# Optimization experiments

Hardware: AMD Instinct MI355X
Metric: run time of the kernel (lower is better)

The kernel has to match this reference:

```python
import jax, jax.numpy as jnp
import numpy as np

BS, SEQ, DK = 4, 4096, 128

def setup_inputs() -> dict:
    key = jax.random.key(0)
    kq, kk, kv = jax.random.split(key, 3)
    q = jax.random.normal(kq, (BS, SEQ, DK), dtype=jnp.float32)
    k = jax.random.normal(kk, (BS, SEQ, DK), dtype=jnp.float32)
    v = jax.random.normal(kv, (BS, SEQ, DK), dtype=jnp.float32)
    return {"q": q, "k": k, "v": v}

def reference(q, k, v):
    d_k = q.shape[-1]
    # scores: [bs, s_q, s_k]
    scaled = jnp.einsum('bqd,bkd->bqk', q, k) / jnp.sqrt(jnp.asarray(d_k, q.dtype))
    # NOTE: original torch code applies softmax over dim=1 (query axis), faithfully reproduced here.
    attn = jax.nn.softmax(scaled, axis=1)
    return jnp.einsum('bqk,bkd->bqd', attn, v)
```

## Files before the change

### kernel.cpp

```cpp
#include <hip/hip_runtime.h>
#include <hip/hip_bf16.h>

#define BS  4
#define SEQ 4096
#define DK  128

#define C1_SCALE (1.4426950408889634f / 11.313708498984761f)

typedef __attribute__((ext_vector_type(8))) short bf16x8;
typedef __attribute__((ext_vector_type(4))) float f32x4;
typedef unsigned short ushort_t;

__device__ inline unsigned pk_bf16(float a, float b) {
    __hip_bfloat162 h = __float22bfloat162_rn(make_float2(a, b));
    union { __hip_bfloat162 h2; unsigned u; } cv;
    cv.h2 = h;
    return cv.u;
}

__device__ inline bf16x8 pk8(float4 a, float4 b) {
    union { bf16x8 v; unsigned u[4]; } r;
    r.u[0] = pk_bf16(a.x, a.y);
    r.u[1] = pk_bf16(a.z, a.w);
    r.u[2] = pk_bf16(b.x, b.y);
    r.u[3] = pk_bf16(b.z, b.w);
    return r.v;
}

__device__ inline void gld_lds16(const ushort_t* g, ushort_t* l) {
    __builtin_amdgcn_global_load_lds(
        (const __attribute__((address_space(1))) unsigned int*)g,
        (__attribute__((address_space(3))) unsigned int*)l,
        16, 0, 0);
}

__global__ __launch_bounds__(256) void cast_qk_sw(
    const float* __restrict__ Q, const float* __restrict__ K,
    ushort_t* __restrict__ Qb, ushort_t* __restrict__ Kb)
{
    const int g = blockIdx.x * 256 + threadIdx.x;
    const int q = g >> 4, ap = g & 15;
    const int a = ap ^ (q & 15);
    const float* src = Q + (size_t)q * DK + a * 8;
    float4 x = *(const float4*)src, y = *(const float4*)(src + 4);
    *(bf16x8*)(Qb + (size_t)g * 8) = pk8(x, y);
    src = K + (size_t)q * DK + a * 8;
    x = *(const float4*)src; y = *(const float4*)(src + 4);
    *(bf16x8*)(Kb + (size_t)g * 8) = pk8(x, y);
}

__global__ __launch_bounds__(256) void sdpa_passA(
    const ushort_t* __restrict__ Qb, const ushort_t* __restrict__ Kb,
    ushort_t* __restrict__ Pg, float* __restrict__ lp)
{
    __shared__ ushort_t Qs[2][4096];
    __shared__ ushort_t Ps[8192];

    const int kt = blockIdx.x, qs = blockIdx.y, b = blockIdx.z;
    const int tid = threadIdx.x;
    const int w = tid >> 6, lane = tid & 63, ln = lane & 15, quad = lane >> 4;

    bf16x8 ka[2][4];
#pragma unroll
    for (int mt = 0; mt < 2; ++mt)
#pragma unroll
        for (int c = 0; c < 4; ++c)
            ka[mt][c] = *(const bf16x8*)(Kb +
                ((size_t)(b * SEQ) + kt * 128 + w * 32 + mt * 16 + ln) * DK +
                (((c * 4 + quad) ^ ln) * 8));

    float ls[2][4] = {};
    const ushort_t* qtb = Qb + ((size_t)(b * SEQ + qs * 512)) * DK;

#define A_DMA(BUF, I)                                                          \
    {                                                                          \
        _Pragma("unroll")                                                      \
        for (int j = 0; j < 2; ++j)                                            \
            gld_lds16(qtb + (size_t)(I) * 4096 + (j * 256 + tid) * 8,          \
                      &Qs[BUF][(j * 256 + w * 64) * 8]);                       \
    }

#define A_CMP(BUF, IT)                                                         \
    {                                                                          \
        bf16x8 qf[2][4];                                                       \
        _Pragma("unroll")                                                      \
        for (int nt = 0; nt < 2; ++nt)                                         \
            _Pragma("unroll")                                                  \
            for (int c = 0; c < 4; ++c)                                        \
                qf[nt][c] = *(const bf16x8*)&Qs[BUF][(nt * 16 + ln) * 128 +    \
                                    (((c * 4 + quad) ^ ln) * 8)];              \
        _Pragma("unroll")                                                      \
        for (int mt = 0; mt < 2; ++mt)                                         \
            _Pragma("unroll")                                                  \
            for (int nt = 0; nt < 2; ++nt) {                                   \
                f32x4 s = {0.f, 0.f, 0.f, 0.f};                                \
                _Pragma("unroll")                                              \
                for (int c = 0; c < 4; ++c)                                    \
                    s = __builtin_amdgcn_mfma_f32_16x16x32_bf16(               \
                        ka[mt][c], qf[nt][c], s, 0, 0, 0);                     \
                float e0 = __builtin_amdgcn_exp2f(C1_SCALE * s[0]);            \
                float e1 = __builtin_amdgcn_exp2f(C1_SCALE * s[1]);            \
                float e2 = __builtin_amdgcn_exp2f(C1_SCALE * s[2]);            \
                float e3 = __builtin_amdgcn_exp2f(C1_SCALE * s[3]);            \
                ls[mt][0] += e0; ls[mt][1] += e1;                              \
                ls[mt][2] += e2; ls[mt][3] += e3;                              \
                uint2 pw; pw.x = pk_bf16(e0, e1); pw.y = pk_bf16(e2, e3);      \
                const int ql = (((IT) & 1) * 32) + nt * 16 + ln;               \
                const int aa = (w & 1) * 4 + mt * 2 + (quad >> 1);             \
                *(uint2*)&Ps[(w >> 1) * 4096 +                                 \
                             (ql * 8 + (aa ^ (ql & 7))) * 8 + (quad & 1) * 4] = pw; \
            }                                                                  \
    }

    A_DMA(0, 0)
    for (int ii = 0; ii < 8; ++ii) {
        const int i0 = 2 * ii;
        __syncthreads();
        A_DMA(1, i0 + 1)
        A_CMP(0, i0)
        __syncthreads();
        if (ii < 7) A_DMA(0, i0 + 2)
        A_CMP(1, i0 + 1)
        __syncthreads();
        {
            const size_t gb = (((size_t)(b * 64 + qs * 8 + ii)) * 64 + kt * 2) * 4096;
#pragma unroll
            for (int j = 0; j < 4; ++j) {
                uint4 t4 = *(const uint4*)&Ps[(j * 256 + tid) * 8];
                *(uint4*)(Pg + gb + (size_t)(j * 256 + tid) * 8) = t4;
            }
        }
    }
#undef A_DMA
#undef A_CMP

#pragma unroll
    for (int mt = 0; mt < 2; ++mt)
#pragma unroll
        for (int r = 0; r < 4; ++r) {
            float vv = ls[mt][r];
            vv += __shfl_xor(vv, 1);
            vv += __shfl_xor(vv, 2);
            vv += __shfl_xor(vv, 4);
            vv += __shfl_xor(vv, 8);
            ls[mt][r] = vv;
        }
    if (ln < 8) {
        int k = kt * 128 + w * 32 + (ln >> 2) * 16 + quad * 4 + (ln & 3);
        lp[((size_t)(qs * BS + b)) * SEQ + k] = ls[ln >> 2][ln & 3];
    }
}

__global__ __launch_bounds__(256) void vb_transpose(
    const float* __restrict__ V, const float* __restrict__ lp,
    ushort_t* __restrict__ VbT)
{
    __shared__ float Vl[64][132];
    __shared__ float Wl[64];

    const int kt = blockIdx.x, b = blockIdx.y;
    const int tid = threadIdx.x;
    const int k0 = kt * 64;
    {
        int r = tid >> 2, sg = tid & 3;
        const float* src = V + ((size_t)(b * SEQ) + k0 + r) * DK + sg * 32;
#pragma unroll
        for (int i = 0; i < 8; ++i)
            *(float4*)&Vl[r][sg * 32 + i * 4] = *(const float4*)(src + i * 4);
    }
    if (tid < 64) {
        float s = 0.f;
#pragma unroll
        for (int qs = 0; qs < 8; ++qs)
            s += lp[((size_t)(qs * BS + b)) * SEQ + k0 + tid];
        Wl[tid] = 1.0f / s;
    }
    __syncthreads();

    const int d = tid >> 1, kh = tid & 1;
    unsigned u[16];
#pragma unroll
    for (int j = 0; j < 16; ++j) {
        int row = kh * 32 + j * 2;
        u[j] = pk_bf16(Vl[row][d] * Wl[row], Vl[row + 1][d] * Wl[row + 1]);
    }
    ushort_t* dst = VbT + ((size_t)(b * DK) + d) * SEQ + k0 + kh * 32;
#pragma unroll
    for (int i = 0; i < 4; ++i) {
        uint4 t4; t4.x = u[i*4]; t4.y = u[i*4+1]; t4.z = u[i*4+2]; t4.w = u[i*4+3];
        *(uint4*)(dst + i * 8) = t4;
    }
}

__global__ __launch_bounds__(256) void sdpa_passB(
    const ushort_t* __restrict__ Pg, const ushort_t* __restrict__ VbT,
    float* __restrict__ Op, float* __restrict__ O, int use_partial)
{
    __shared__ ushort_t Pt[2][4096];

    const int g  = blockIdx.x;
    const int qt = blockIdx.y;
    const int ks = g >> 2, b = g & 3;
    const int tid = threadIdx.x;
    const int w = tid >> 6, lane = tid & 63, ln = lane & 15, quad = lane >> 4;

    f32x4 acc[4][2];
#pragma unroll
    for (int i = 0; i < 4; ++i)
#pragma unroll
        for (int j = 0; j < 2; ++j) acc[i][j] = (f32x4){0.f, 0.f, 0.f, 0.f};

    const ushort_t* ptile = Pg + (((size_t)(b * 64 + qt)) * 64 + ks * 16) * 4096;
    const ushort_t* vfp = VbT + ((size_t)(b * DK) + w * 32 + ln) * SEQ + ks * 1024 + quad * 8;

    bf16x8 vf0[4], vf1[4];

#define B_DMA(BUF, I)                                                          \
    {                                                                          \
        const ushort_t* src = ptile + (size_t)(I) * 4096;                      \
        _Pragma("unroll")                                                      \
        for (int j = 0; j < 2; ++j)                                            \
            gld_lds16(src + (j * 256 + tid) * 8,                               \
                      &Pt[BUF][(j * 256 + w * 64) * 8]);                       \
    }

#define B_PRV(VF, I)                                                           \
    {                                                                          \
        _Pragma("unroll")                                                      \
        for (int dt = 0; dt < 2; ++dt)                                         \
            _Pragma("unroll")                                                  \
            for (int kc = 0; kc < 2; ++kc)                                     \
                VF[kc * 2 + dt] = *(const bf16x8*)(vfp +                       \
                    (size_t)dt * 16 * SEQ + (I) * 64 + kc * 32);               \
    }

#define B_PV(BUF, VF)                                                          \
    {                                                                          \
        _Pragma("unroll")                                                      \
        for (int kc = 0; kc < 2; ++kc) {                                       \
            bf16x8 pa[4];                                                      \
            _Pragma("unroll")                                                  \
            for (int qf2 = 0; qf2 < 4; ++qf2)                                  \
                pa[qf2] = *(const bf16x8*)&Pt[BUF][(qf2 * 16 + ln) * 64 +      \
                                    (((kc * 4 + quad) ^ (ln & 7)) * 8)];       \
            _Pragma("unroll")                                                  \
            for (int qf2 = 0; qf2 < 4; ++qf2)                                  \
                _Pragma("unroll")                                              \
                for (int dt = 0; dt < 2; ++dt)                                 \
                    acc[qf2][dt] = __builtin_amdgcn_mfma_f32_16x16x32_bf16(    \
                        pa[qf2], VF[kc * 2 + dt], acc[qf2][dt], 0, 0, 0);      \
        }                                                                      \
    }

    B_DMA(0, 0)
    B_PRV(vf0, 0)
    for (int ii = 0; ii < 8; ++ii) {
        const int i0 = 2 * ii;
        __syncthreads();
        B_DMA(1, i0 + 1)
        B_PRV(vf1, i0 + 1)
        B_PV(0, vf0)
        __syncthreads();
        if (ii < 7) {
            B_DMA(0, i0 + 2)
            B_PRV(vf0, i0 + 2)
        }
        B_PV(1, vf1)
    }
#undef B_DMA
#undef B_PRV
#undef B_PV

    if (use_partial) {
        float* dst = Op + (size_t)ks * (BS * SEQ * DK) +
                     ((size_t)(b * SEQ) + qt * 64 + quad * 4) * DK + w * 32 + ln;
#pragma unroll
        for (int qf2 = 0; qf2 < 4; ++qf2)
#pragma unroll
            for (int dt = 0; dt < 2; ++dt)
#pragma unroll
                for (int r = 0; r < 4; ++r)
                    dst[((size_t)(qf2 * 16 + r)) * DK + dt * 16] = acc[qf2][dt][r];
    } else {
#pragma unroll
        for (int qf2 = 0; qf2 < 4; ++qf2)
#pragma unroll
            for (int dt = 0; dt < 2; ++dt)
#pragma unroll
                for (int r = 0; r < 4; ++r)
                    atomicAdd(&O[((size_t)(b * SEQ) + qt * 64 + qf2 * 16 + quad * 4 + r) * DK +
                                 w * 32 + dt * 16 + ln], acc[qf2][dt][r]);
    }
}

__global__ __launch_bounds__(256) void reduce4(
    const float* __restrict__ Op, float* __restrict__ O)
{
    const size_t N = (size_t)BS * SEQ * DK;
    size_t i = ((size_t)blockIdx.x * 256 + threadIdx.x) * 4;
    float4 a0 = *(const float4*)(Op + i);
    float4 a1 = *(const float4*)(Op + N + i);
    float4 a2 = *(const float4*)(Op + 2 * N + i);
    float4 a3 = *(const float4*)(Op + 3 * N + i);
    float4 r;
    r.x = a0.x + a1.x + a2.x + a3.x;
    r.y = a0.y + a1.y + a2.y + a3.y;
    r.z = a0.z + a1.z + a2.z + a3.z;
    r.w = a0.w + a1.w + a2.w + a3.w;
    *(float4*)(O + i) = r;
}

__global__ __launch_bounds__(256) void sdpa_lsum_fb(
    const ushort_t* __restrict__ Qb, const ushort_t* __restrict__ Kb,
    float* __restrict__ lp)
{
    const int kt = blockIdx.x, qs = blockIdx.y, b = blockIdx.z;
    const int tid = threadIdx.x;
    const int w = tid >> 6, lane = tid & 63, ln = lane & 15, quad = lane >> 4;

    bf16x8 ka[2][4];
#pragma unroll
    for (int mt = 0; mt < 2; ++mt)
#pragma unroll
        for (int c = 0; c < 4; ++c)
            ka[mt][c] = *(const bf16x8*)(Kb +
                ((size_t)(b * SEQ) + kt * 128 + w * 32 + mt * 16 + ln) * DK +
                (((c * 4 + quad) ^ ln) * 8));

    float ls[2][4] = {};
    const ushort_t* qbase = Qb + ((size_t)(b * SEQ) + qs * 512 + ln) * DK;
    bf16x8 qf0[2][4], qf1[2][4];

#define L_PRE(QF, IT)                                                          \
    {                                                                          \
        _Pragma("unroll")                                                      \
        for (int nt = 0; nt < 2; ++nt)                                         \
            _Pragma("unroll")                                                  \
            for (int c = 0; c < 4; ++c)                                        \
                QF[nt][c] = *(const bf16x8*)(qbase +                           \
                    ((size_t)((IT) * 32 + nt * 16)) * DK +                     \
                    (((c * 4 + quad) ^ ln) * 8));                              \
    }
#define L_CMP(QF)                                                              \
    {                                                                          \
        _Pragma("unroll")                                                      \
        for (int mt = 0; mt < 2; ++mt)                                         \
            _Pragma("unroll")                                                  \
            for (int nt = 0; nt < 2; ++nt) {                                   \
                f32x4 s = {0.f, 0.f, 0.f, 0.f};                                \
                _Pragma("unroll")                                              \
                for (int c = 0; c < 4; ++c)                                    \
                    s = __builtin_amdgcn_mfma_f32_16x16x32_bf16(               \
                        ka[mt][c], QF[nt][c], s, 0, 0, 0);                     \
                _Pragma("unroll")                                              \
                for (int r = 0; r < 4; ++r)                                    \
                    ls[mt][r] += __builtin_amdgcn_exp2f(C1_SCALE * s[r]);      \
            }                                                                  \
    }
    L_PRE(qf0, 0)
    for (int ii = 0; ii < 8; ++ii) {
        const int i0 = 2 * ii;
        L_PRE(qf1, i0 + 1)
        L_CMP(qf0)
        if (ii < 7) L_PRE(qf0, i0 + 2)
        L_CMP(qf1)
    }
#undef L_PRE
#undef L_CMP

#pragma unroll
    for (int mt = 0; mt < 2; ++mt)
#pragma unroll
        for (int r = 0; r < 4; ++r) {
            float vv = ls[mt][r];
            vv += __shfl_xor(vv, 1);
            vv += __shfl_xor(vv, 2);
            vv += __shfl_xor(vv, 4);
            vv += __shfl_xor(vv, 8);
            ls[mt][r] = vv;
        }
    if (ln < 8) {
        int k = kt * 128 + w * 32 + (ln >> 2) * 16 + quad * 4 + (ln & 3);
        lp[((size_t)(qs * BS + b)) * SEQ + k] = ls[ln >> 2][ln & 3];
    }
}

__global__ __launch_bounds__(256) void sdpa_out_fb(
    const ushort_t* __restrict__ Qb, const ushort_t* __restrict__ Kb,
    const ushort_t* __restrict__ VbT, float* __restrict__ O)
{
    __shared__ ushort_t Pt[2][64 * 64];

    const int g  = blockIdx.x;
    const int qt = blockIdx.y;
    const int ks = g >> 2, b = g & 3;
    const int tid = threadIdx.x;
    const int w = tid >> 6, lane = tid & 63, ln = lane & 15, quad = lane >> 4;

    bf16x8 qa[4][4];
#pragma unroll
    for (int nt = 0; nt < 4; ++nt)
#pragma unroll
        for (int c = 0; c < 4; ++c)
            qa[c][nt] = *(const bf16x8*)(Qb +
                ((size_t)(b * SEQ) + qt * 64 + nt * 16 + ln) * DK +
                (((c * 4 + quad) ^ ln) * 8));

    f32x4 acc[4][2];
#pragma unroll
    for (int i = 0; i < 4; ++i)
#pragma unroll
        for (int j = 0; j < 2; ++j) acc[i][j] = (f32x4){0.f, 0.f, 0.f, 0.f};

    const ushort_t* kfp = Kb + ((size_t)(b * SEQ) + ks * 1024 + w * 16 + ln) * DK;
    const ushort_t* vfp = VbT + ((size_t)(b * DK) + w * 32 + ln) * SEQ + ks * 1024 + quad * 8;

    bf16x8 kf0[4], kf1[4], vf0[4], vf1[4];

#define QK_PHASE(P, KF)                                                        \
    {                                                                          \
        _Pragma("unroll")                                                      \
        for (int nt = 0; nt < 4; ++nt) {                                       \
            f32x4 s = {0.f, 0.f, 0.f, 0.f};                                    \
            _Pragma("unroll")                                                  \
            for (int c = 0; c < 4; ++c)                                        \
                s = __builtin_amdgcn_mfma_f32_16x16x32_bf16(KF[c], qa[c][nt], s, 0, 0, 0); \
            uint2 pw;                                                          \
            pw.x = pk_bf16(__builtin_amdgcn_exp2f(C1_SCALE * s[0]),            \
                           __builtin_amdgcn_exp2f(C1_SCALE * s[1]));           \
            pw.y = pk_bf16(__builtin_amdgcn_exp2f(C1_SCALE * s[2]),            \
                           __builtin_amdgcn_exp2f(C1_SCALE * s[3]));           \
            const int q = nt * 16 + ln;                                        \
            const int a16 = w * 2 + (quad >> 1);                               \
            *(uint2*)&Pt[P][q * 64 + ((a16 ^ (q & 7)) * 8) + (quad & 1) * 4] = pw; \
        }                                                                      \
    }
#define PREFETCH(KF, VF, I1)                                                   \
    {                                                                          \
        _Pragma("unroll")                                                      \
        for (int c = 0; c < 4; ++c)                                            \
            KF[c] = *(const bf16x8*)(kfp + (size_t)(I1) * 64 * DK +            \
                                     (((c * 4 + quad) ^ ln) * 8));             \
        _Pragma("unroll")                                                      \
        for (int dt = 0; dt < 2; ++dt)                                         \
            _Pragma("unroll")                                                  \
            for (int kc = 0; kc < 2; ++kc)                                     \
                VF[kc * 2 + dt] = *(const bf16x8*)(vfp +                       \
                    (size_t)dt * 16 * SEQ + (size_t)(I1) * 64 + kc * 32);      \
    }
#define PV_PHASE(P, VF)                                                        \
    {                                                                          \
        _Pragma("unroll")                                                      \
        for (int kc = 0; kc < 2; ++kc) {                                       \
            bf16x8 pa[4];                                                      \
            _Pragma("unroll")                                                  \
            for (int qf2 = 0; qf2 < 4; ++qf2)                                  \
                pa[qf2] = *(const bf16x8*)&Pt[P][(qf2 * 16 + ln) * 64 +        \
                                    (((kc * 4 + quad) ^ (ln & 7)) * 8)];       \
            _Pragma("unroll")                                                  \
            for (int qf2 = 0; qf2 < 4; ++qf2)                                  \
                _Pragma("unroll")                                              \
                for (int dt = 0; dt < 2; ++dt)                                 \
                    acc[qf2][dt] = __builtin_amdgcn_mfma_f32_16x16x32_bf16(    \
                        pa[qf2], VF[kc * 2 + dt], acc[qf2][dt], 0, 0, 0);      \
        }                                                                      \
    }

#pragma unroll
    for (int c = 0; c < 4; ++c)
        kf0[c] = *(const bf16x8*)(kfp + (((c * 4 + quad) ^ ln) * 8));
#pragma unroll
    for (int dt = 0; dt < 2; ++dt)
#pragma unroll
        for (int kc = 0; kc < 2; ++kc)
            vf0[kc * 2 + dt] = *(const bf16x8*)(vfp + (size_t)dt * 16 * SEQ + kc * 32);

    for (int ii = 0; ii < 8; ++ii) {
        const int i0 = 2 * ii;
        PREFETCH(kf1, vf1, i0 + 1)
        QK_PHASE(0, kf0)
        __syncthreads();
        PV_PHASE(0, vf0)
        if (ii < 7) PREFETCH(kf0, vf0, i0 + 2)
        QK_PHASE(1, kf1)
        __syncthreads();
        PV_PHASE(1, vf1)
    }
#undef QK_PHASE
#undef PREFETCH
#undef PV_PHASE

#pragma unroll
    for (int qf2 = 0; qf2 < 4; ++qf2)
#pragma unroll
        for (int dt = 0; dt < 2; ++dt)
#pragma unroll
            for (int r = 0; r < 4; ++r)
                atomicAdd(&O[((size_t)(b * SEQ) + qt * 64 + qf2 * 16 + quad * 4 + r) * DK +
                             w * 32 + dt * 16 + ln], acc[qf2][dt][r]);
}

extern "C" void kernel_launch(void* const* d_in, const int* in_sizes, int n_in,
                              void* d_out, int out_size, void* d_ws, size_t ws_size,
                              hipStream_t stream) {
    const float* q = (const float*)d_in[0];
    const float* k = (const float*)d_in[1];
    const float* v = (const float*)d_in[2];
    float* out = (float*)d_out;

    const size_t QKV = (size_t)BS * SEQ * DK;
    float*    lp  = (float*)d_ws;
    ushort_t* Qb  = (ushort_t*)((char*)d_ws + (1 << 20));
    ushort_t* Kb  = Qb + QKV;
    ushort_t* VbT = Kb + QKV;
    ushort_t* Pg  = VbT + QKV;
    float*    Op  = (float*)(Pg + (size_t)BS * SEQ * SEQ);

    const size_t need1 = (1u << 20) + 3 * QKV * 2 + (size_t)BS * SEQ * SEQ * 2;
    const size_t need2 = need1 + 4 * QKV * sizeof(float);

    cast_qk_sw<<<dim3(BS * SEQ * 16 / 256), 256, 0, stream>>>(q, k, Qb, Kb);

    if (ws_size >= need2) {
        sdpa_passA  <<<dim3(32, 8, 4), 256, 0, stream>>>(Qb, Kb, Pg, lp);
        vb_transpose<<<dim3(64, 4),    256, 0, stream>>>(v, lp, VbT);
        sdpa_passB  <<<dim3(16, 64),   256, 0, stream>>>(Pg, VbT, Op, out, 1);
        reduce4     <<<dim3(BS * SEQ * DK / 4 / 256), 256, 0, stream>>>(Op, out);
    } else if (ws_size >= need1) {
        hipMemsetAsync(out, 0, QKV * sizeof(float), stream);
        sdpa_passA  <<<dim3(32, 8, 4), 256, 0, stream>>>(Qb, Kb, Pg, lp);
        vb_transpose<<<dim3(64, 4),    256, 0, stream>>>(v, lp, VbT);
        sdpa_passB  <<<dim3(16, 64),   256, 0, stream>>>(Pg, VbT, (float*)Pg, out, 0);
    } else {
        hipMemsetAsync(out, 0, QKV * sizeof(float), stream);
        sdpa_lsum_fb<<<dim3(32, 8, 4), 256, 0, stream>>>(Qb, Kb, lp);
        vb_transpose<<<dim3(64, 4),    256, 0, stream>>>(v, lp, VbT);
        sdpa_out_fb <<<dim3(16, 64),   256, 0, stream>>>(Qb, Kb, VbT, out);
    }
}
```

Measured before the change: 172.5 us.

## Recompute QK^T exponentials in output pass instead of materializing P in global memory

Pass A no longer writes the full bf16 exp(QK^T) matrix (BS*SEQ*SEQ) to global memory; it only computes column sums. The output pass recomputes QK^T and the exponentials from Qb/Kb with MFMA and stages P tiles in LDS before the PV product, keeping the partial-sum reduce path. This trades roughly 128 MB of global writes plus reads for doubling the QK matmul and exp work.

```diff
diff --git a/kernel.cpp b/kernel.cpp
--- a/kernel.cpp
+++ b/kernel.cpp
@@ -25,13 +25,6 @@
     r.u[2] = pk_bf16(b.x, b.y);
     r.u[3] = pk_bf16(b.z, b.w);
     return r.v;
-}
-
-__device__ inline void gld_lds16(const ushort_t* g, ushort_t* l) {
-    __builtin_amdgcn_global_load_lds(
-        (const __attribute__((address_space(1))) unsigned int*)g,
-        (__attribute__((address_space(3))) unsigned int*)l,
-        16, 0, 0);
 }
 
 __global__ __launch_bounds__(256) void cast_qk_sw(
@@ -49,13 +42,10 @@
     *(bf16x8*)(Kb + (size_t)g * 8) = pk8(x, y);
 }
 
-__global__ __launch_bounds__(256) void sdpa_passA(
+__global__ __launch_bounds__(256) void sdpa_lsum(
     const ushort_t* __restrict__ Qb, const ushort_t* __restrict__ Kb,
-    ushort_t* __restrict__ Pg, float* __restrict__ lp)
-{
-    __shared__ ushort_t Qs[2][4096];
-    __shared__ ushort_t Ps[8192];
-
+    float* __restrict__ lp)
+{
     const int kt = blockIdx.x, qs = blockIdx.y, b = blockIdx.z;
     const int tid = threadIdx.x;
     const int w = tid >> 6, lane = tid & 63, ln = lane & 15, quad = lane >> 4;
@@ -70,25 +60,21 @@
                 (((c * 4 + quad) ^ ln) * 8));
 
     float ls[2][4] = {};
-    const ushort_t* qtb = Qb + ((size_t)(b * SEQ + qs * 512)) * DK;
-
-#define A_DMA(BUF, I)                                                          \
-    {                                                                          \
-        _Pragma("unroll")                                                      \
-        for (int j = 0; j < 2; ++j)                                            \
-            gld_lds16(qtb + (size_t)(I) * 4096 + (j * 256 + tid) * 8,          \
-                      &Qs[BUF][(j * 256 + w * 64) * 8]);                       \
-    }
-
-#define A_CMP(BUF, IT)                                                         \
-    {                                                                          \
-        bf16x8 qf[2][4];                                                       \
+    const ushort_t* qbase = Qb + ((size_t)(b * SEQ) + qs * 512 + ln) * DK;
+    bf16x8 qf0[2][4], qf1[2][4];
+
+#define L_PRE(QF, IT)                                                          \
+    {                                                                          \
         _Pragma("unroll")                                                      \
         for (int nt = 0; nt < 2; ++nt)                                         \
             _Pragma("unroll")                                                  \
             for (int c = 0; c < 4; ++c)                                        \
-                qf[nt][c] = *(const bf16x8*)&Qs[BUF][(nt * 16 + ln) * 128 +    \
-                                    (((c * 4 + quad) ^ ln) * 8)];              \
+                QF[nt][c] = *(const bf16x8*)(qbase +                           \
+                    ((size_t)((IT) * 32 + nt * 16)) * DK +                     \
+                    (((c * 4 + quad) ^ ln) * 8));                              \
+    }
+#define L_CMP(QF)                                                              \
+    {                                                                          \
         _Pragma("unroll")                                                      \
         for (int mt = 0; mt < 2; ++mt)                                         \
             _Pragma("unroll")                                                  \
@@ -97,42 +83,22 @@
                 _Pragma("unroll")                                              \
                 for (int c = 0; c < 4; ++c)                                    \
                     s = __builtin_amdgcn_mfma_f32_16x16x32_bf16(               \
-                        ka[mt][c], qf[nt][c], s, 0, 0, 0);                     \
-                float e0 = __builtin_amdgcn_exp2f(C1_SCALE * s[0]);            \
-                float e1 = __builtin_amdgcn_exp2f(C1_SCALE * s[1]);            \
-                float e2 = __builtin_amdgcn_exp2f(C1_SCALE * s[2]);            \
-                float e3 = __builtin_amdgcn_exp2f(C1_SCALE * s[3]);            \
-                ls[mt][0] += e0; ls[mt][1] += e1;                              \
-                ls[mt][2] += e2; ls[mt][3] += e3;                              \
-                uint2 pw; pw.x = pk_bf16(e0, e1); pw.y = pk_bf16(e2, e3);      \
-                const int ql = (((IT) & 1) * 32) + nt * 16 + ln;               \
-                const int aa = (w & 1) * 4 + mt * 2 + (quad >> 1);             \
-                *(uint2*)&Ps[(w >> 1) * 4096 +                                 \
-                             (ql * 8 + (aa ^ (ql & 7))) * 8 + (quad & 1) * 4] = pw; \
+                        ka[mt][c], QF[nt][c], s, 0, 0, 0);                     \
+                _Pragma("unroll")                                              \
+                for (int r = 0; r < 4; ++r)                                    \
+                    ls[mt][r] += __builtin_amdgcn_exp2f(C1_SCALE * s[r]);      \
             }                                                                  \
     }
-
-    A_DMA(0, 0)
+    L_PRE(qf0, 0)
     for (int ii = 0; ii < 8; ++ii) {
         const int i0 = 2 * ii;
-        __syncthreads();
-        A_DMA(1, i0 + 1)
-        A_CMP(0, i0)
-        __syncthreads();
-        if (ii < 7) A_DMA(0, i0 + 2)
-        A_CMP(1, i0 + 1)
-        __syncthreads();
-        {
-            const size_t gb = (((size_t)(b * 64 + qs * 8 + ii)) * 64 + kt * 2) * 4096;
-#pragma unroll
-            for (int j = 0; j < 4; ++j) {
-                uint4 t4 = *(const uint4*)&Ps[(j * 256 + tid) * 8];
-                *(uint4*)(Pg + gb + (size_t)(j * 256 + tid) * 8) = t4;
-            }
-        }
-    }
-#undef A_DMA
-#undef A_CMP
+        L_PRE(qf1, i0 + 1)
+        L_CMP(qf0)
+        if (ii < 7) L_PRE(qf0, i0 + 2)
+        L_CMP(qf1)
+    }
+#undef L_PRE
+#undef L_CMP
 
 #pragma unroll
     for (int mt = 0; mt < 2; ++mt)
@@ -192,11 +158,12 @@
     }
 }
 
-__global__ __launch_bounds__(256) void sdpa_passB(
-    const ushort_t* __restrict__ Pg, const ushort_t* __restrict__ VbT,
+__global__ __launch_bounds__(256) void sdpa_out(
+    const ushort_t* __restrict__ Qb, const ushort_t* __restrict__ Kb,
+    const ushort_t* __restrict__ VbT,
     float* __restrict__ Op, float* __restrict__ O, int use_partial)
 {
-    __shared__ ushort_t Pt[2][4096];
+    __shared__ ushort_t Pt[2][64 * 64];
 
     const int g  = blockIdx.x;
     const int qt = blockIdx.y;
@@ -204,44 +171,65 @@
     const int tid = threadIdx.x;
     const int w = tid >> 6, lane = tid & 63, ln = lane & 15, quad = lane >> 4;
 
+    bf16x8 qa[4][4];
+#pragma unroll
+    for (int nt = 0; nt < 4; ++nt)
+#pragma unroll
+        for (int c = 0; c < 4; ++c)
+            qa[c][nt] = *(const bf16x8*)(Qb +
+                ((size_t)(b * SEQ) + qt * 64 + nt * 16 + ln) * DK +
+                (((c * 4 + quad) ^ ln) * 8));
+
     f32x4 acc[4][2];
 #pragma unroll
     for (int i = 0; i < 4; ++i)
 #pragma unroll
         for (int j = 0; j < 2; ++j) acc[i][j] = (f32x4){0.f, 0.f, 0.f, 0.f};
 
-    const ushort_t* ptile = Pg + (((size_t)(b * 64 + qt)) * 64 + ks * 16) * 4096;
+    const ushort_t* kfp = Kb + ((size_t)(b * SEQ) + ks * 1024 + w * 16 + ln) * DK;
     const ushort_t* vfp = VbT + ((size_t)(b * DK) + w * 32 + ln) * SEQ + ks * 1024 + quad * 8;
 
-    bf16x8 vf0[4], vf1[4];
-
-#define B_DMA(BUF, I)                                                          \
-    {                                                                          \
-        const ushort_t* src = ptile + (size_t)(I) * 4096;                      \
-        _Pragma("unroll")                                                      \
-        for (int j = 0; j < 2; ++j)                                            \
-            gld_lds16(src + (j * 256 + tid) * 8,                               \
-                      &Pt[BUF][(j * 256 + w * 64) * 8]);                       \
-    }
-
-#define B_PRV(VF, I)                                                           \
-    {                                                                          \
+    bf16x8 kf0[4], kf1[4], vf0[4], vf1[4];
+
+#define QK_PHASE(P, KF)                                                        \
+    {                                                                          \
+        _Pragma("unroll")                                                      \
+        for (int nt = 0; nt < 4; ++nt) {                                       \
+            f32x4 s = {0.f, 0.f, 0.f, 0.f};                                    \
+            _Pragma("unroll")                                                  \
+            for (int c = 0; c < 4; ++c)                                        \
+                s = __builtin_amdgcn_mfma_f32_16x16x32_bf16(KF[c], qa[c][nt], s, 0, 0, 0); \
+            uint2 pw;                                                          \
+            pw.x = pk_bf16(__builtin_amdgcn_exp2f(C1_SCALE * s[0]),            \
+                           __builtin_amdgcn_exp2f(C1_SCALE * s[1]));           \
+            pw.y = pk_bf16(__builtin_amdgcn_exp2f(C1_SCALE * s[2]),            \
+                           __builtin_amdgcn_exp2f(C1_SCALE * s[3]));           \
+            const int q = nt * 16 + ln;                                        \
+            const int a16 = w * 2 + (quad >> 1);                               \
+            *(uint2*)&Pt[P][q * 64 + ((a16 ^ (q & 7)) * 8) + (quad & 1) * 4] = pw; \
+        }                                                                      \
+    }
+#define PREFETCH(KF, VF, I1)                                                   \
+    {                                                                          \
+        _Pragma("unroll")                                                      \
+        for (int c = 0; c < 4; ++c)                                            \
+            KF[c] = *(const bf16x8*)(kfp + (size_t)(I1) * 64 * DK +            \
+                                     (((c * 4 + quad) ^ ln) * 8));             \
         _Pragma("unroll")                                                      \
         for (int dt = 0; dt < 2; ++dt)                                         \
             _Pragma("unroll")                                                  \
             for (int kc = 0; kc < 2; ++kc)                                     \
                 VF[kc * 2 + dt] = *(const bf16x8*)(vfp +                       \
-                    (size_t)dt * 16 * SEQ + (I) * 64 + kc * 32);               \
-    }
-
-#define B_PV(BUF, VF)                                                          \
+                    (size_t)dt * 16 * SEQ + (size_t)(I1) * 64 + kc * 32);      \
+    }
+#define PV_PHASE(P, VF)                                                        \
     {                                                                          \
         _Pragma("unroll")                                                      \
         for (int kc = 0; kc < 2; ++kc) {                                       \
             bf16x8 pa[4];                                                      \
             _Pragma("unroll")                                                  \
             for (int qf2 = 0; qf2 < 4; ++qf2)                                  \
-                pa[qf2] = *(const bf16x8*)&Pt[BUF][(qf2 * 16 + ln) * 64 +      \
+                pa[qf2] = *(const bf16x8*)&Pt[P][(qf2 * 16 + ln) * 64 +        \
                                     (((kc * 4 + quad) ^ (ln & 7)) * 8)];       \
             _Pragma("unroll")                                                  \
             for (int qf2 = 0; qf2 < 4; ++qf2)                                  \
@@ -252,27 +240,32 @@
         }                                                                      \
     }
 
-    B_DMA(0, 0)
-    B_PRV(vf0, 0)
+#pragma unroll
+    for (int c = 0; c < 4; ++c)
+        kf0[c] = *(const bf16x8*)(kfp + (((c * 4 + quad) ^ ln) * 8));
+#pragma unroll
+    for (int dt = 0; dt < 2; ++dt)
+#pragma unroll
+        for (int kc = 0; kc < 2; ++kc)
+            vf0[kc * 2 + dt] = *(const bf16x8*)(vfp + (size_t)dt * 16 * SEQ + kc * 32);
+
     for (int ii = 0; ii < 8; ++ii) {
         const int i0 = 2 * ii;
+        PREFETCH(kf1, vf1, i0 + 1)
+        QK_PHASE(0, kf0)
         __syncthreads();
-        B_DMA(1, i0 + 1)
-        B_PRV(vf1, i0 + 1)
-        B_PV(0, vf0)
+        PV_PHASE(0, vf0)
+        if (ii < 7) PREFETCH(kf0, vf0, i0 + 2)
+        QK_PHASE(1, kf1)
         __syncthreads();
-        if (ii < 7) {
-            B_DMA(0, i0 + 2)
-            B_PRV(vf0, i0 + 2)
-        }
-        B_PV(1, vf1)
-    }
-#undef B_DMA
-#undef B_PRV
-#undef B_PV
+        PV_PHASE(1, vf1)
+    }
+#undef QK_PHASE
+#undef PREFETCH
+#undef PV_PHASE
 
     if (use_partial) {
-        float* dst = Op + (size_t)ks * (BS * SEQ * DK) +
+        float* dst = Op + (size_t)ks * ((size_t)BS * SEQ * DK) +
                      ((size_t)(b * SEQ) + qt * 64 + quad * 4) * DK + w * 32 + ln;
 #pragma unroll
         for (int qf2 = 0; qf2 < 4; ++qf2)
@@ -310,196 +303,6 @@
     *(float4*)(O + i) = r;
 }
 
-__global__ __launch_bounds__(256) void sdpa_lsum_fb(
-    const ushort_t* __restrict__ Qb, const ushort_t* __restrict__ Kb,
-    float* __restrict__ lp)
-{
-    const int kt = blockIdx.x, qs = blockIdx.y, b = blockIdx.z;
-    const int tid = threadIdx.x;
-    const int w = tid >> 6, lane = tid & 63, ln = lane & 15, quad = lane >> 4;
-
-    bf16x8 ka[2][4];
-#pragma unroll
-    for (int mt = 0; mt < 2; ++mt)
-#pragma unroll
-        for (int c = 0; c < 4; ++c)
-            ka[mt][c] = *(const bf16x8*)(Kb +
-                ((size_t)(b * SEQ) + kt * 128 + w * 32 + mt * 16 + ln) * DK +
-                (((c * 4 + quad) ^ ln) * 8));
-
-    float ls[2][4] = {};
-    const ushort_t* qbase = Qb + ((size_t)(b * SEQ) + qs * 512 + ln) * DK;
-    bf16x8 qf0[2][4], qf1[2][4];
-
-#define L_PRE(QF, IT)                                                          \
-    {                                                                          \
-        _Pragma("unroll")                                                      \
-        for (int nt = 0; nt < 2; ++nt)                                         \
-            _Pragma("unroll")                                                  \
-            for (int c = 0; c < 4; ++c)                                        \
-                QF[nt][c] = *(const bf16x8*)(qbase +                           \
-                    ((size_t)((IT) * 32 + nt * 16)) * DK +                     \
-                    (((c * 4 + quad) ^ ln) * 8));                              \
-    }
-#define L_CMP(QF)                                                              \
-    {                                                                          \
-        _Pragma("unroll")                                                      \
-        for (int mt = 0; mt < 2; ++mt)                                         \
-            _Pragma("unroll")                                                  \
-            for (int nt = 0; nt < 2; ++nt) {                                   \
-                f32x4 s = {0.f, 0.f, 0.f, 0.f};                                \
-                _Pragma("unroll")                                              \
-                for (int c = 0; c < 4; ++c)                                    \
-                    s = __builtin_amdgcn_mfma_f32_16x16x32_bf16(               \
-                        ka[mt][c], QF[nt][c], s, 0, 0, 0);                     \
-                _Pragma("unroll")                                              \
-                for (int r = 0; r < 4; ++r)                                    \
-                    ls[mt][r] += __builtin_amdgcn_exp2f(C1_SCALE * s[r]);      \
-            }                                                                  \
-    }
-    L_PRE(qf0, 0)
-    for (int ii = 0; ii < 8; ++ii) {
-        const int i0 = 2 * ii;
-        L_PRE(qf1, i0 + 1)
-        L_CMP(qf0)
-        if (ii < 7) L_PRE(qf0, i0 + 2)
-        L_CMP(qf1)
-    }
-#undef L_PRE
-#undef L_CMP
-
-#pragma unroll
-    for (int mt = 0; mt < 2; ++mt)
-#pragma unroll
-        for (int r = 0; r < 4; ++r) {
-            float vv = ls[mt][r];
-            vv += __shfl_xor(vv, 1);
-            vv += __shfl_xor(vv, 2);
-            vv += __shfl_xor(vv, 4);
-            vv += __shfl_xor(vv, 8);
-            ls[mt][r] = vv;
-        }
-    if (ln < 8) {
-        int k = kt * 128 + w * 32 + (ln >> 2) * 16 + quad * 4 + (ln & 3);
-        lp[((size_t)(qs * BS + b)) * SEQ + k] = ls[ln >> 2][ln & 3];
-    }
-}
-
-__global__ __launch_bounds__(256) void sdpa_out_fb(
-    const ushort_t* __restrict__ Qb, const ushort_t* __restrict__ Kb,
-    const ushort_t* __restrict__ VbT, float* __restrict__ O)
-{
-    __shared__ ushort_t Pt[2][64 * 64];
-
-    const int g  = blockIdx.x;
-    const int qt = blockIdx.y;
-    const int ks = g >> 2, b = g & 3;
-    const int tid = threadIdx.x;
-    const int w = tid >> 6, lane = tid & 63, ln = lane & 15, quad = lane >> 4;
-
-    bf16x8 qa[4][4];
-#pragma unroll
-    for (int nt = 0; nt < 4; ++nt)
-#pragma unroll
-        for (int c = 0; c < 4; ++c)
-            qa[c][nt] = *(const bf16x8*)(Qb +
-                ((size_t)(b * SEQ) + qt * 64 + nt * 16 + ln) * DK +
-                (((c * 4 + quad) ^ ln) * 8));
-
-    f32x4 acc[4][2];
-#pragma unroll
-    for (int i = 0; i < 4; ++i)
-#pragma unroll
-        for (int j = 0; j < 2; ++j) acc[i][j] = (f32x4){0.f, 0.f, 0.f, 0.f};
-
-    const ushort_t* kfp = Kb + ((size_t)(b * SEQ) + ks * 1024 + w * 16 + ln) * DK;
-    const ushort_t* vfp = VbT + ((size_t)(b * DK) + w * 32 + ln) * SEQ + ks * 1024 + quad * 8;
-
-    bf16x8 kf0[4], kf1[4], vf0[4], vf1[4];
-
-#define QK_PHASE(P, KF)                                                        \
-    {                                                                          \
-        _Pragma("unroll")                                                      \
-        for (int nt = 0; nt < 4; ++nt) {                                       \
-            f32x4 s = {0.f, 0.f, 0.f, 0.f};                                    \
-            _Pragma("unroll")                                                  \
-            for (int c = 0; c < 4; ++c)                                        \
-                s = __builtin_amdgcn_mfma_f32_16x16x32_bf16(KF[c], qa[c][nt], s, 0, 0, 0); \
-            uint2 pw;                                                          \
-            pw.x = pk_bf16(__builtin_amdgcn_exp2f(C1_SCALE * s[0]),            \
-                           __builtin_amdgcn_exp2f(C1_SCALE * s[1]));           \
-            pw.y = pk_bf16(__builtin_amdgcn_exp2f(C1_SCALE * s[2]),            \
-                           __builtin_amdgcn_exp2f(C1_SCALE * s[3]));           \
-            const int q = nt * 16 + ln;                                        \
-            const int a16 = w * 2 + (quad >> 1);                               \
-            *(uint2*)&Pt[P][q * 64 + ((a16 ^ (q & 7)) * 8) + (quad & 1) * 4] = pw; \
-        }                                                                      \
-    }
-#define PREFETCH(KF, VF, I1)                                                   \
-    {                                                                          \
-        _Pragma("unroll")                                                      \
-        for (int c = 0; c < 4; ++c)                                            \
-            KF[c] = *(const bf16x8*)(kfp + (size_t)(I1) * 64 * DK +            \
-                                     (((c * 4 + quad) ^ ln) * 8));             \
-        _Pragma("unroll")                                                      \
-        for (int dt = 0; dt < 2; ++dt)                                         \
-            _Pragma("unroll")                                                  \
-            for (int kc = 0; kc < 2; ++kc)                                     \
-                VF[kc * 2 + dt] = *(const bf16x8*)(vfp +                       \
-                    (size_t)dt * 16 * SEQ + (size_t)(I1) * 64 + kc * 32);      \
-    }
-#define PV_PHASE(P, VF)                                                        \
-    {                                                                          \
-        _Pragma("unroll")                                                      \
-        for (int kc = 0; kc < 2; ++kc) {                                       \
-            bf16x8 pa[4];                                                      \
-            _Pragma("unroll")                                                  \
-            for (int qf2 = 0; qf2 < 4; ++qf2)                                  \
-                pa[qf2] = *(const bf16x8*)&Pt[P][(qf2 * 16 + ln) * 64 +        \
-                                    (((kc * 4 + quad) ^ (ln & 7)) * 8)];       \
-            _Pragma("unroll")                                                  \
-            for (int qf2 = 0; qf2 < 4; ++qf2)                                  \
-                _Pragma("unroll")                                              \
-                for (int dt = 0; dt < 2; ++dt)                                 \
-                    acc[qf2][dt] = __builtin_amdgcn_mfma_f32_16x16x32_bf16(    \
-                        pa[qf2], VF[kc * 2 + dt], acc[qf2][dt], 0, 0, 0);      \
-        }                                                                      \
-    }
-
-#pragma unroll
-    for (int c = 0; c < 4; ++c)
-        kf0[c] = *(const bf16x8*)(kfp + (((c * 4 + quad) ^ ln) * 8));
-#pragma unroll
-    for (int dt = 0; dt < 2; ++dt)
-#pragma unroll
-        for (int kc = 0; kc < 2; ++kc)
-            vf0[kc * 2 + dt] = *(const bf16x8*)(vfp + (size_t)dt * 16 * SEQ + kc * 32);
-
-    for (int ii = 0; ii < 8; ++ii) {
-        const int i0 = 2 * ii;
-        PREFETCH(kf1, vf1, i0 + 1)
-        QK_PHASE(0, kf0)
-        __syncthreads();
-        PV_PHASE(0, vf0)
-        if (ii < 7) PREFETCH(kf0, vf0, i0 + 2)
-        QK_PHASE(1, kf1)
-        __syncthreads();
-        PV_PHASE(1, vf1)
-    }
-#undef QK_PHASE
-#undef PREFETCH
-#undef PV_PHASE
-
-#pragma unroll
-    for (int qf2 = 0; qf2 < 4; ++qf2)
-#pragma unroll
-        for (int dt = 0; dt < 2; ++dt)
-#pragma unroll
-            for (int r = 0; r < 4; ++r)
-                atomicAdd(&O[((size_t)(b * SEQ) + qt * 64 + qf2 * 16 + quad * 4 + r) * DK +
-                             w * 32 + dt * 16 + ln], acc[qf2][dt][r]);
-}
-
 extern "C" void kernel_launch(void* const* d_in, const int* in_sizes, int n_in,
                               void* d_out, int out_size, void* d_ws, size_t ws_size,
                               hipStream_t stream) {
@@ -513,28 +316,19 @@
     ushort_t* Qb  = (ushort_t*)((char*)d_ws + (1 << 20));
     ushort_t* Kb  = Qb + QKV;
     ushort_t* VbT = Kb + QKV;
-    ushort_t* Pg  = VbT + QKV;
-    float*    Op  = (float*)(Pg + (size_t)BS * SEQ * SEQ);
-
-    const size_t need1 = (1u << 20) + 3 * QKV * 2 + (size_t)BS * SEQ * SEQ * 2;
-    const size_t need2 = need1 + 4 * QKV * sizeof(float);
+    float*    Op  = (float*)(VbT + QKV);
+
+    const size_t need_p = (1u << 20) + 3 * QKV * 2 + 4 * QKV * sizeof(float);
 
     cast_qk_sw<<<dim3(BS * SEQ * 16 / 256), 256, 0, stream>>>(q, k, Qb, Kb);
-
-    if (ws_size >= need2) {
-        sdpa_passA  <<<dim3(32, 8, 4), 256, 0, stream>>>(Qb, Kb, Pg, lp);
-        vb_transpose<<<dim3(64, 4),    256, 0, stream>>>(v, lp, VbT);
-        sdpa_passB  <<<dim3(16, 64),   256, 0, stream>>>(Pg, VbT, Op, out, 1);
-        reduce4     <<<dim3(BS * SEQ * DK / 4 / 256), 256, 0, stream>>>(Op, out);
-    } else if (ws_size >= need1) {
-        hipMemsetAsync(out, 0, QKV * sizeof(float), stream);
-        sdpa_passA  <<<dim3(32, 8, 4), 256, 0, stream>>>(Qb, Kb, Pg, lp);
-        vb_transpose<<<dim3(64, 4),    256, 0, stream>>>(v, lp, VbT);
-        sdpa_passB  <<<dim3(16, 64),   256, 0, stream>>>(Pg, VbT, (float*)Pg, out, 0);
+    sdpa_lsum  <<<dim3(32, 8, 4), 256, 0, stream>>>(Qb, Kb, lp);
+    vb_transpose<<<dim3(64, 4),   256, 0, stream>>>(v, lp, VbT);
+
+    if (ws_size >= need_p) {
+        sdpa_out<<<dim3(16, 64), 256, 0, stream>>>(Qb, Kb, VbT, Op, out, 1);
+        reduce4 <<<dim3(BS * SEQ * DK / 4 / 256), 256, 0, stream>>>(Op, out);
     } else {
         hipMemsetAsync(out, 0, QKV * sizeof(float), stream);
-        sdpa_lsum_fb<<<dim3(32, 8, 4), 256, 0, stream>>>(Qb, Kb, lp);
-        vb_transpose<<<dim3(64, 4),    256, 0, stream>>>(v, lp, VbT);
-        sdpa_out_fb <<<dim3(16, 64),   256, 0, stream>>>(Qb, Kb, VbT, out);
-    }
-}
+        sdpa_out<<<dim3(16, 64), 256, 0, stream>>>(Qb, Kb, VbT, nullptr, out, 0);
+    }
+}
```

After: 183.7 us. 1.07x slower.
